# Optimization experiments

Hardware: AMD Instinct MI355X
Metric: run time of the kernel (lower is better)

The kernel has to match this reference:

```python
import jax, jax.numpy as jnp
import numpy as np
import math

B, D_MODEL, SEQ_LEN, EMB_DIM, ORDER = 4, 1024, 4096, 5, 64


def setup_inputs() -> dict:
    key = jax.random.key(0)
    ks = jax.random.split(key, 12)
    L = SEQ_LEN
    # PositionalEmbedding: z = [t, Re(e^{-i f w}), Im(e^{-i f w})]
    t = jnp.linspace(0.0, 1.0, L)[None, :, None]                      # [1,L,1]
    bands = (EMB_DIM - 1) // 2
    t_rescaled = jnp.linspace(0.0, L - 1, L)[None, :, None]           # [1,L,1]
    w = 2 * math.pi * t_rescaled / L
    f = jnp.linspace(1e-4, bands - 1, bands)[None, None]              # [1,1,bands]
    zc = jnp.exp(-1j * f * w.astype(jnp.complex64))                   # [1,L,bands]
    z = jnp.concatenate([t, zc.real, zc.imag], axis=-1)               # [1,L,EMB_DIM]
    # ExponentialModulation deltas (fast_decay_pct=0.3, slow_decay_pct=1.5, target=0.01)
    max_decay = math.log(0.01) / 0.3
    min_decay = math.log(0.01) / 1.5
    deltas = jnp.linspace(min_decay, max_decay, D_MODEL)[None, None]  # [1,1,D]
    s = 0.1  # small init scale for MLP weights
    return {
        "x": jax.random.normal(ks[0], (B, D_MODEL, SEQ_LEN), jnp.float32),
        "L": SEQ_LEN,
        "z": z.astype(jnp.float32),
        "t": t.astype(jnp.float32),
        "deltas": deltas.astype(jnp.float32),
        "W1": jax.random.normal(ks[1], (ORDER, EMB_DIM), jnp.float32) * s,
        "b1": jax.random.normal(ks[2], (ORDER,), jnp.float32) * s,
        "freq": jnp.ones((1, ORDER), jnp.float32),  # Sin freq, w=1
        "W2": jax.random.normal(ks[3], (ORDER, ORDER), jnp.float32) * s,
        "b2": jax.random.normal(ks[4], (ORDER,), jnp.float32) * s,
        "W3": jax.random.normal(ks[5], (ORDER, ORDER), jnp.float32) * s,
        "b3": jax.random.normal(ks[6], (ORDER,), jnp.float32) * s,
        "W4": jax.random.normal(ks[7], (D_MODEL, ORDER), jnp.float32) * s,
        "bias": jax.random.normal(ks[8], (D_MODEL,), jnp.float32),
    }


def reference(x, L, z, t, deltas, W1, b1, freq, W2, b2, W3, b3, W4, bias):
    # --- implicit filter MLP: z [1,L,E] -> k [1,L,D] ---
    zL, tL = z[:, :L], t[:, :L]
    h = jnp.sin(freq * (jnp.einsum('ble,oe->blo', zL, W1) + b1))
    h = jnp.sin(freq * (jnp.einsum('blo,po->blp', h, W2) + b2))
    h = jnp.sin(freq * (jnp.einsum('blo,po->blp', h, W3) + b3))
    h = jnp.einsum('blo,do->bld', h, W4)                # [1,L,D], no bias
    # --- exponential modulation ---
    decay = jnp.exp(-tL * jnp.abs(deltas))              # [1,L,D]
    h = h * decay
    k = h[0].T                                          # [D, L] per-channel filters
    # --- FFT causal conv: irfft(rfft(u)*rfft(k)/n, norm='forward') == plain circular conv on 2L ---
    n = 2 * L
    u_f = jnp.fft.rfft(x, n=n)                          # [B,D,L+1] complex
    k_f = jnp.fft.rfft(k, n=n)                          # [D,L+1]
    y = jnp.fft.irfft(u_f * k_f, n=n)[..., :L]          # [B,D,L]
    out = y + x * bias[:, None]                         # D.unsqueeze(-1) bias term, gelu=False
    return out.astype(x.dtype)
```

## Files before the change

kernel.cpp:

```cpp
#include <hip/hip_runtime.h>
#include <math.h>


#define PAD(i) ((i) + ((i) >> 4))
#define TWO_PI 6.2831853071795864769f

typedef float2 cplx;

__device__ __forceinline__ cplx cmul(cplx a, cplx b) {
    return make_float2(a.x * b.x - a.y * b.y, a.x * b.y + a.y * b.x);
}

__device__ __forceinline__ void dft8(cplx v[8], float sgn) {
    cplx t;
    t = v[1]; v[1] = v[4]; v[4] = t;
    t = v[3]; v[3] = v[6]; v[6] = t;
#pragma unroll
    for (int i = 0; i < 8; i += 2) {
        cplx a = v[i], b = v[i + 1];
        v[i]     = make_float2(a.x + b.x, a.y + b.y);
        v[i + 1] = make_float2(a.x - b.x, a.y - b.y);
    }
#pragma unroll
    for (int i = 0; i < 8; i += 4) {
        cplx a = v[i], b = v[i + 2];
        v[i]     = make_float2(a.x + b.x, a.y + b.y);
        v[i + 2] = make_float2(a.x - b.x, a.y - b.y);
        cplx c1 = v[i + 1], d = v[i + 3];
        cplx dt = make_float2(-sgn * d.y, sgn * d.x);
        v[i + 1] = make_float2(c1.x + dt.x, c1.y + dt.y);
        v[i + 3] = make_float2(c1.x - dt.x, c1.y - dt.y);
    }
    const float C = 0.70710678118654752440f;
    cplx a, b, bt;
    a = v[0]; b = v[4];
    v[0] = make_float2(a.x + b.x, a.y + b.y);
    v[4] = make_float2(a.x - b.x, a.y - b.y);
    a = v[1]; b = v[5]; bt = cmul(b, make_float2(C, sgn * C));
    v[1] = make_float2(a.x + bt.x, a.y + bt.y);
    v[5] = make_float2(a.x - bt.x, a.y - bt.y);
    a = v[2]; b = v[6]; bt = make_float2(-sgn * b.y, sgn * b.x);
    v[2] = make_float2(a.x + bt.x, a.y + bt.y);
    v[6] = make_float2(a.x - bt.x, a.y - bt.y);
    a = v[3]; b = v[7]; bt = cmul(b, make_float2(-C, sgn * C));
    v[3] = make_float2(a.x + bt.x, a.y + bt.y);
    v[7] = make_float2(a.x - bt.x, a.y - bt.y);
}

__device__ __forceinline__ void twiddle_powers(float ang, cplx w[8]) {
    float s, c;
    __sincosf(ang, &s, &c);
    w[1] = make_float2(c, s);
    w[2] = cmul(w[1], w[1]);
    w[3] = cmul(w[2], w[1]);
    w[4] = cmul(w[2], w[2]);
    w[5] = cmul(w[4], w[1]);
    w[6] = cmul(w[3], w[3]);
    w[7] = cmul(w[4], w[3]);
}

template <int NS>
__device__ __forceinline__ void fft_pass_ip(cplx* buf, int j, float sgn) {
    cplx v[8];
#pragma unroll
    for (int r = 0; r < 8; r++) v[r] = buf[PAD(j + (r << 9))];
    if (NS > 1) {
        int jm = j & (NS - 1);
        float ang = sgn * (TWO_PI / (float)(NS * 8)) * (float)jm;
        cplx w[8];
        twiddle_powers(ang, w);
#pragma unroll
        for (int r = 1; r < 8; r++) v[r] = cmul(v[r], w[r]);
    }
    dft8(v, sgn);
    __syncthreads();
    int jm2 = j & (NS - 1);
    int base = ((j & ~(NS - 1)) << 3) + jm2;
#pragma unroll
    for (int r = 0; r < 8; r++) buf[PAD(base + r * NS)] = v[r];
    __syncthreads();
}

__device__ __forceinline__ void fft_pass1_fwd_regs(cplx* buf, int j, const cplx xv[4]) {
    cplx v[8];
#pragma unroll
    for (int r = 0; r < 4; r++) v[r] = xv[r];
#pragma unroll
    for (int r = 4; r < 8; r++) v[r] = make_float2(0.f, 0.f);
    dft8(v, -1.0f);
#pragma unroll
    for (int r = 0; r < 8; r++) buf[PAD(8 * j + r)] = v[r];
    __syncthreads();
}

__global__ __launch_bounds__(256) void mlp_kernel(
    const float* __restrict__ zin, const float* __restrict__ W1,
    const float* __restrict__ b1, const float* __restrict__ freq,
    const float* __restrict__ W2, const float* __restrict__ b2,
    const float* __restrict__ W3, const float* __restrict__ b3,
    float* __restrict__ h3T) {
    __shared__ float hs1[64][64];
    __shared__ float hs2[64][64];
    int tid = threadIdx.x;
    int l = tid & 63, w = tid >> 6;
    int lg = blockIdx.x * 64 + l;

    float zf[5];
#pragma unroll
    for (int e = 0; e < 5; e++) zf[e] = zin[lg * 5 + e];

#pragma unroll
    for (int i = 0; i < 16; i++) {
        int o = w * 16 + i;
        float a = b1[o];
#pragma unroll
        for (int e = 0; e < 5; e++) a += W1[o * 5 + e] * zf[e];
        hs1[o][l] = __sinf(freq[o] * a);
    }
    __syncthreads();

    float acc[16];
#pragma unroll
    for (int i = 0; i < 16; i++) acc[i] = b2[w * 16 + i];
#pragma unroll 8
    for (int o = 0; o < 64; o++) {
        float hv = hs1[o][l];
#pragma unroll
        for (int i = 0; i < 16; i++) acc[i] += W2[(w * 16 + i) * 64 + o] * hv;
    }
#pragma unroll
    for (int i = 0; i < 16; i++)
        hs2[w * 16 + i][l] = __sinf(freq[w * 16 + i] * acc[i]);
    __syncthreads();

#pragma unroll
    for (int i = 0; i < 16; i++) acc[i] = b3[w * 16 + i];
#pragma unroll 8
    for (int o = 0; o < 64; o++) {
        float hv = hs2[o][l];
#pragma unroll
        for (int i = 0; i < 16; i++) acc[i] += W3[(w * 16 + i) * 64 + o] * hv;
    }
#pragma unroll
    for (int i = 0; i < 16; i++)
        h3T[(size_t)(w * 16 + i) * 4096 + lg] = __sinf(freq[w * 16 + i] * acc[i]);
}

__global__ __launch_bounds__(256) void kgemm_kernel(
    const float* __restrict__ h3T, const float* __restrict__ W4,
    const float* __restrict__ tvec, const float* __restrict__ deltas,
    float* __restrict__ kout) {
    int lt = blockIdx.x & 3;
    int dt = blockIdx.x >> 2;
    int l0 = lt * 1024 + threadIdx.x * 4;
    float4 acc[16];
#pragma unroll
    for (int i = 0; i < 16; i++) acc[i] = make_float4(0.f, 0.f, 0.f, 0.f);
#pragma unroll 8
    for (int o = 0; o < 64; o++) {
        float4 h = *(const float4*)(h3T + (size_t)o * 4096 + l0);
#pragma unroll
        for (int i = 0; i < 16; i++) {
            float wv = W4[(size_t)(dt * 16 + i) * 64 + o];
            acc[i].x += wv * h.x; acc[i].y += wv * h.y;
            acc[i].z += wv * h.z; acc[i].w += wv * h.w;
        }
    }
    float4 tl = *(const float4*)(tvec + l0);
#pragma unroll
    for (int i = 0; i < 16; i++) {
        int d = dt * 16 + i;
        float da = fabsf(deltas[d]);
        float4 o;
        o.x = acc[i].x * __expf(-tl.x * da);
        o.y = acc[i].y * __expf(-tl.y * da);
        o.z = acc[i].z * __expf(-tl.z * da);
        o.w = acc[i].w * __expf(-tl.w * da);
        *(float4*)(kout + (size_t)d * 4096 + l0) = o;
    }
}

__global__ __launch_bounds__(512) void filter_fft_kernel(
    const float* __restrict__ kin, float2* __restrict__ Kf) {
    __shared__ cplx buf[4352];
    int d = blockIdx.x, t = threadIdx.x;

    const cplx* k2 = (const cplx*)(kin + (size_t)d * 4096);
    cplx xv[4];
#pragma unroll
    for (int r = 0; r < 4; r++) xv[r] = k2[t + (r << 9)];
    fft_pass1_fwd_regs(buf, t, xv);
    fft_pass_ip<8>(buf, t, -1.0f);
    fft_pass_ip<64>(buf, t, -1.0f);
    fft_pass_ip<512>(buf, t, -1.0f);

    const float scale = 1.0f / 4096.0f;
    float sb, cb;
    __sincosf(-TWO_PI * (float)t * (1.0f / 8192.0f), &sb, &cb);
    cplx wt = make_float2(cb, sb);
    const cplx WC0 = make_float2(1.0f, 0.0f);
    const cplx WC1 = make_float2(0.92387953251128675613f, -0.38268343236508977173f);
    const cplx WC2 = make_float2(0.70710678118654752440f, -0.70710678118654752440f);
    const cplx WC3 = make_float2(0.38268343236508977173f, -0.92387953251128675613f);
    float2* KfRow = Kf + (size_t)d * 4104;
#pragma unroll
    for (int i = 0; i < 4; i++) {
        int k = t + (i << 9);
        cplx wk = (i == 0) ? cmul(wt, WC0) : (i == 1) ? cmul(wt, WC1)
                 : (i == 2) ? cmul(wt, WC2) : cmul(wt, WC3);
        if (k == 0) {
            cplx z0 = buf[PAD(0)];
            KfRow[0]    = make_float2((z0.x + z0.y) * scale, 0.f);
            KfRow[4096] = make_float2((z0.x - z0.y) * scale, 0.f);
            cplx zm = buf[PAD(2048)];
            KfRow[2048] = make_float2(zm.x * scale, -zm.y * scale);
        } else {
            int k2i = 4096 - k;
            cplx Zk = buf[PAD(k)], Zq = buf[PAD(k2i)];
            cplx Fe = make_float2(0.5f * (Zk.x + Zq.x), 0.5f * (Zk.y - Zq.y));
            cplx Fo = make_float2(0.5f * (Zk.y + Zq.y), -0.5f * (Zk.x - Zq.x));
            cplx WFo = cmul(wk, Fo);
            KfRow[k]   = make_float2((Fe.x + WFo.x) * scale, (Fe.y + WFo.y) * scale);
            KfRow[k2i] = make_float2((Fe.x - WFo.x) * scale, -(Fe.y - WFo.y) * scale);
        }
    }
}

__global__ __launch_bounds__(512) void conv_kernel(
    const float* __restrict__ x, const float2* __restrict__ Kf,
    const float* __restrict__ bias, float* __restrict__ out) {
    __shared__ cplx buf[4352];
    int rid = blockIdx.x;
    int d = rid & 1023;
    int t = threadIdx.x;

    const cplx* x2 = (const cplx*)(x + (size_t)rid * 4096);
    cplx xv[4];
#pragma unroll
    for (int r = 0; r < 4; r++) xv[r] = x2[t + (r << 9)];
    fft_pass1_fwd_regs(buf, t, xv);
    fft_pass_ip<8>(buf, t, -1.0f);
    fft_pass_ip<64>(buf, t, -1.0f);
    fft_pass_ip<512>(buf, t, -1.0f);

    const float2* KfRow = Kf + (size_t)d * 4104;
    float sb, cb;
    __sincosf(-TWO_PI * (float)t * (1.0f / 8192.0f), &sb, &cb);
    cplx wt = make_float2(cb, sb);
    const cplx WC0 = make_float2(1.0f, 0.0f);
    const cplx WC1 = make_float2(0.92387953251128675613f, -0.38268343236508977173f);
    const cplx WC2 = make_float2(0.70710678118654752440f, -0.70710678118654752440f);
    const cplx WC3 = make_float2(0.38268343236508977173f, -0.92387953251128675613f);
#pragma unroll
    for (int i = 0; i < 4; i++) {
        int k = t + (i << 9);
        cplx wk = (i == 0) ? cmul(wt, WC0) : (i == 1) ? cmul(wt, WC1)
                 : (i == 2) ? cmul(wt, WC2) : cmul(wt, WC3);
        if (k == 0) {
            cplx z0 = buf[PAD(0)];
            float U0 = z0.x + z0.y;
            float UN = z0.x - z0.y;
            float Y0 = U0 * KfRow[0].x;
            float YN = UN * KfRow[4096].x;
            buf[PAD(0)] = make_float2(0.5f * (Y0 + YN), 0.5f * (Y0 - YN));
            cplx zm = buf[PAD(2048)];
            cplx Um = make_float2(zm.x, -zm.y);
            cplx Ym = cmul(Um, KfRow[2048]);
            buf[PAD(2048)] = make_float2(Ym.x, -Ym.y);
        } else {
            int k2i = 4096 - k;
            cplx Zk = buf[PAD(k)], Zq = buf[PAD(k2i)];
            cplx K1 = KfRow[k], K2 = KfRow[k2i];
            cplx Fe = make_float2(0.5f * (Zk.x + Zq.x), 0.5f * (Zk.y - Zq.y));
            cplx Fo = make_float2(0.5f * (Zk.y + Zq.y), -0.5f * (Zk.x - Zq.x));
            cplx WFo = cmul(wk, Fo);
            cplx U1 = make_float2(Fe.x + WFo.x, Fe.y + WFo.y);
            cplx U2 = make_float2(Fe.x - WFo.x, -(Fe.y - WFo.y));
            cplx Y1 = cmul(U1, K1);
            cplx Y2 = cmul(U2, K2);
            cplx FeY = make_float2(0.5f * (Y1.x + Y2.x), 0.5f * (Y1.y - Y2.y));
            cplx T   = make_float2(0.5f * (Y1.x - Y2.x), 0.5f * (Y1.y + Y2.y));
            cplx FoY = cmul(make_float2(wk.x, -wk.y), T);
            buf[PAD(k)]   = make_float2(FeY.x - FoY.y, FeY.y + FoY.x);
            buf[PAD(k2i)] = make_float2(FeY.x + FoY.y, FoY.x - FeY.y);
        }
    }
    __syncthreads();

    fft_pass_ip<1>(buf, t, 1.0f);
    fft_pass_ip<8>(buf, t, 1.0f);
    fft_pass_ip<64>(buf, t, 1.0f);
    {
        cplx v[8];
#pragma unroll
        for (int r = 0; r < 8; r++) v[r] = buf[PAD(t + (r << 9))];
        float ang = (TWO_PI / 4096.0f) * (float)t;
        cplx w[8];
        twiddle_powers(ang, w);
#pragma unroll
        for (int r = 1; r < 8; r++) v[r] = cmul(v[r], w[r]);
        dft8(v, 1.0f);
        float bd = bias[d];
        cplx* o2 = (cplx*)(out + (size_t)rid * 4096);
#pragma unroll
        for (int r = 0; r < 4; r++) {
            int m = t + (r << 9);
            cplx o;
            o.x = v[r].x + xv[r].x * bd;
            o.y = v[r].y + xv[r].y * bd;
            o2[m] = o;
        }
    }
}

extern "C" void kernel_launch(void* const* d_in, const int* in_sizes, int n_in,
                              void* d_out, int out_size, void* d_ws, size_t ws_size,
                              hipStream_t stream) {
    const float* x      = (const float*)d_in[0];
    const float* zin    = (const float*)d_in[2];
    const float* tvec   = (const float*)d_in[3];
    const float* deltas = (const float*)d_in[4];
    const float* W1     = (const float*)d_in[5];
    const float* b1     = (const float*)d_in[6];
    const float* freq   = (const float*)d_in[7];
    const float* W2     = (const float*)d_in[8];
    const float* b2     = (const float*)d_in[9];
    const float* W3     = (const float*)d_in[10];
    const float* b3     = (const float*)d_in[11];
    const float* W4     = (const float*)d_in[12];
    const float* bias   = (const float*)d_in[13];
    float* out = (float*)d_out;

    float*  h3T = (float*)d_ws;
    float2* Kf  = (float2*)((char*)d_ws + (size_t)64 * 4096 * sizeof(float));
    float* kbuf = out + (size_t)3072 * 4096;

    mlp_kernel<<<64, 256, 0, stream>>>(zin, W1, b1, freq, W2, b2, W3, b3, h3T);
    kgemm_kernel<<<256, 256, 0, stream>>>(h3T, W4, tvec, deltas, kbuf);
    filter_fft_kernel<<<1024, 512, 0, stream>>>(kbuf, Kf);
    conv_kernel<<<4096, 512, 0, stream>>>(x, Kf, bias, out);
}
```

Before: 244.1 us.

## Fuse filter FFT into conv kernel, one block per channel looping over batch

Merges the filter FFT and convolution kernels into one. Each block handles one channel: it computes the filter spectrum once, keeps it in registers, then loops over the four batch rows, prefetching the next row's input while the current row's FFTs run. This removes the Kf round trip through global memory and one kernel launch. The shared-memory FFT addressing is also rewritten to use precomputed padded pointers with constant offsets. In exchange the grid shrinks from 4096 blocks to 1024 and each block runs serially over the batch, which lowers parallelism, and register pressure rises.

```diff
diff --git a/kernel.cpp b/kernel.cpp
--- a/kernel.cpp
+++ b/kernel.cpp
@@ -60,10 +60,11 @@
 }
 
 template <int NS>
-__device__ __forceinline__ void fft_pass_ip(cplx* buf, int j, float sgn) {
+__device__ __forceinline__ void fft_pass_ip(cplx* __restrict__ buf, int j, float sgn) {
+    cplx* rp = buf + (j + (j >> 4));
     cplx v[8];
 #pragma unroll
-    for (int r = 0; r < 8; r++) v[r] = buf[PAD(j + (r << 9))];
+    for (int r = 0; r < 8; r++) v[r] = rp[544 * r];
     if (NS > 1) {
         int jm = j & (NS - 1);
         float ang = sgn * (TWO_PI / (float)(NS * 8)) * (float)jm;
@@ -74,22 +75,31 @@
     }
     dft8(v, sgn);
     __syncthreads();
-    int jm2 = j & (NS - 1);
-    int base = ((j & ~(NS - 1)) << 3) + jm2;
-#pragma unroll
-    for (int r = 0; r < 8; r++) buf[PAD(base + r * NS)] = v[r];
-    __syncthreads();
-}
-
-__device__ __forceinline__ void fft_pass1_fwd_regs(cplx* buf, int j, const cplx xv[4]) {
+    int base = ((j & ~(NS - 1)) << 3) + (j & (NS - 1));
+    cplx* wp = buf + (base + (base >> 4));
+#pragma unroll
+    for (int r = 0; r < 8; r++) {
+        const int off = (NS == 1) ? r
+                      : (NS == 8) ? (8 * r + (r >> 1))
+                      : (NS == 64) ? (68 * r)
+                      : (544 * r);
+        wp[off] = v[r];
+    }
+    __syncthreads();
+}
+
+__device__ __forceinline__ void fft_pass1_fwd_regs(cplx* __restrict__ buf, int j,
+                                                   const cplx xv[4]) {
     cplx v[8];
 #pragma unroll
     for (int r = 0; r < 4; r++) v[r] = xv[r];
 #pragma unroll
     for (int r = 4; r < 8; r++) v[r] = make_float2(0.f, 0.f);
     dft8(v, -1.0f);
-#pragma unroll
-    for (int r = 0; r < 8; r++) buf[PAD(8 * j + r)] = v[r];
+    int b8 = 8 * j;
+    cplx* wp = buf + (b8 + (b8 >> 4));
+#pragma unroll
+    for (int r = 0; r < 8; r++) wp[r] = v[r];
     __syncthreads();
 }
 
@@ -180,136 +190,132 @@
     }
 }
 
-__global__ __launch_bounds__(512) void filter_fft_kernel(
-    const float* __restrict__ kin, float2* __restrict__ Kf) {
+__global__ __launch_bounds__(512) void convf_kernel(
+    const float* __restrict__ x, const float* __restrict__ kin,
+    const float* __restrict__ bias, float* __restrict__ out) {
     __shared__ cplx buf[4352];
-    int d = blockIdx.x, t = threadIdx.x;
-
-    const cplx* k2 = (const cplx*)(kin + (size_t)d * 4096);
-    cplx xv[4];
-#pragma unroll
-    for (int r = 0; r < 4; r++) xv[r] = k2[t + (r << 9)];
-    fft_pass1_fwd_regs(buf, t, xv);
-    fft_pass_ip<8>(buf, t, -1.0f);
-    fft_pass_ip<64>(buf, t, -1.0f);
-    fft_pass_ip<512>(buf, t, -1.0f);
-
-    const float scale = 1.0f / 4096.0f;
+    int d = blockIdx.x;
+    int t = threadIdx.x;
+
     float sb, cb;
     __sincosf(-TWO_PI * (float)t * (1.0f / 8192.0f), &sb, &cb);
-    cplx wt = make_float2(cb, sb);
-    const cplx WC0 = make_float2(1.0f, 0.0f);
-    const cplx WC1 = make_float2(0.92387953251128675613f, -0.38268343236508977173f);
-    const cplx WC2 = make_float2(0.70710678118654752440f, -0.70710678118654752440f);
-    const cplx WC3 = make_float2(0.38268343236508977173f, -0.92387953251128675613f);
-    float2* KfRow = Kf + (size_t)d * 4104;
+    cplx wk[4];
+    wk[0] = make_float2(cb, sb);
+    wk[1] = cmul(wk[0], make_float2(0.92387953251128675613f, -0.38268343236508977173f));
+    wk[2] = cmul(wk[0], make_float2(0.70710678118654752440f, -0.70710678118654752440f));
+    wk[3] = cmul(wk[0], make_float2(0.38268343236508977173f, -0.92387953251128675613f));
+
+    cplx* rb  = buf + (t + (t >> 4));
+    cplx* qb2 = buf + (((4096 - t) + ((4096 - t) >> 4)) - 1632);
+
+    {
+        const cplx* k2 = (const cplx*)(kin + (size_t)d * 4096);
+        cplx kv[4];
+#pragma unroll
+        for (int r = 0; r < 4; r++) kv[r] = k2[t + (r << 9)];
+        fft_pass1_fwd_regs(buf, t, kv);
+        fft_pass_ip<8>(buf, t, -1.0f);
+        fft_pass_ip<64>(buf, t, -1.0f);
+        fft_pass_ip<512>(buf, t, -1.0f);
+    }
+    const float scale = 1.0f / 4096.0f;
+    cplx Kk[4], Kq[4], Km = make_float2(0.f, 0.f);
 #pragma unroll
     for (int i = 0; i < 4; i++) {
-        int k = t + (i << 9);
-        cplx wk = (i == 0) ? cmul(wt, WC0) : (i == 1) ? cmul(wt, WC1)
-                 : (i == 2) ? cmul(wt, WC2) : cmul(wt, WC3);
-        if (k == 0) {
-            cplx z0 = buf[PAD(0)];
-            KfRow[0]    = make_float2((z0.x + z0.y) * scale, 0.f);
-            KfRow[4096] = make_float2((z0.x - z0.y) * scale, 0.f);
+        if (t == 0 && i == 0) {
+            cplx z0 = buf[0];
+            Kk[0] = make_float2((z0.x + z0.y) * scale, (z0.x - z0.y) * scale);
             cplx zm = buf[PAD(2048)];
-            KfRow[2048] = make_float2(zm.x * scale, -zm.y * scale);
+            Km = make_float2(zm.x * scale, -zm.y * scale);
+            Kq[0] = make_float2(0.f, 0.f);
         } else {
-            int k2i = 4096 - k;
-            cplx Zk = buf[PAD(k)], Zq = buf[PAD(k2i)];
+            cplx Zk = rb[544 * i];
+            cplx Zq = qb2[544 * (3 - i)];
             cplx Fe = make_float2(0.5f * (Zk.x + Zq.x), 0.5f * (Zk.y - Zq.y));
             cplx Fo = make_float2(0.5f * (Zk.y + Zq.y), -0.5f * (Zk.x - Zq.x));
-            cplx WFo = cmul(wk, Fo);
-            KfRow[k]   = make_float2((Fe.x + WFo.x) * scale, (Fe.y + WFo.y) * scale);
-            KfRow[k2i] = make_float2((Fe.x - WFo.x) * scale, -(Fe.y - WFo.y) * scale);
-        }
-    }
-}
-
-__global__ __launch_bounds__(512) void conv_kernel(
-    const float* __restrict__ x, const float2* __restrict__ Kf,
-    const float* __restrict__ bias, float* __restrict__ out) {
-    __shared__ cplx buf[4352];
-    int rid = blockIdx.x;
-    int d = rid & 1023;
-    int t = threadIdx.x;
-
-    const cplx* x2 = (const cplx*)(x + (size_t)rid * 4096);
-    cplx xv[4];
-#pragma unroll
-    for (int r = 0; r < 4; r++) xv[r] = x2[t + (r << 9)];
-    fft_pass1_fwd_regs(buf, t, xv);
-    fft_pass_ip<8>(buf, t, -1.0f);
-    fft_pass_ip<64>(buf, t, -1.0f);
-    fft_pass_ip<512>(buf, t, -1.0f);
-
-    const float2* KfRow = Kf + (size_t)d * 4104;
-    float sb, cb;
-    __sincosf(-TWO_PI * (float)t * (1.0f / 8192.0f), &sb, &cb);
-    cplx wt = make_float2(cb, sb);
-    const cplx WC0 = make_float2(1.0f, 0.0f);
-    const cplx WC1 = make_float2(0.92387953251128675613f, -0.38268343236508977173f);
-    const cplx WC2 = make_float2(0.70710678118654752440f, -0.70710678118654752440f);
-    const cplx WC3 = make_float2(0.38268343236508977173f, -0.92387953251128675613f);
-#pragma unroll
-    for (int i = 0; i < 4; i++) {
-        int k = t + (i << 9);
-        cplx wk = (i == 0) ? cmul(wt, WC0) : (i == 1) ? cmul(wt, WC1)
-                 : (i == 2) ? cmul(wt, WC2) : cmul(wt, WC3);
-        if (k == 0) {
-            cplx z0 = buf[PAD(0)];
-            float U0 = z0.x + z0.y;
-            float UN = z0.x - z0.y;
-            float Y0 = U0 * KfRow[0].x;
-            float YN = UN * KfRow[4096].x;
-            buf[PAD(0)] = make_float2(0.5f * (Y0 + YN), 0.5f * (Y0 - YN));
-            cplx zm = buf[PAD(2048)];
-            cplx Um = make_float2(zm.x, -zm.y);
-            cplx Ym = cmul(Um, KfRow[2048]);
-            buf[PAD(2048)] = make_float2(Ym.x, -Ym.y);
-        } else {
-            int k2i = 4096 - k;
-            cplx Zk = buf[PAD(k)], Zq = buf[PAD(k2i)];
-            cplx K1 = KfRow[k], K2 = KfRow[k2i];
-            cplx Fe = make_float2(0.5f * (Zk.x + Zq.x), 0.5f * (Zk.y - Zq.y));
-            cplx Fo = make_float2(0.5f * (Zk.y + Zq.y), -0.5f * (Zk.x - Zq.x));
-            cplx WFo = cmul(wk, Fo);
-            cplx U1 = make_float2(Fe.x + WFo.x, Fe.y + WFo.y);
-            cplx U2 = make_float2(Fe.x - WFo.x, -(Fe.y - WFo.y));
-            cplx Y1 = cmul(U1, K1);
-            cplx Y2 = cmul(U2, K2);
-            cplx FeY = make_float2(0.5f * (Y1.x + Y2.x), 0.5f * (Y1.y - Y2.y));
-            cplx T   = make_float2(0.5f * (Y1.x - Y2.x), 0.5f * (Y1.y + Y2.y));
-            cplx FoY = cmul(make_float2(wk.x, -wk.y), T);
-            buf[PAD(k)]   = make_float2(FeY.x - FoY.y, FeY.y + FoY.x);
-            buf[PAD(k2i)] = make_float2(FeY.x + FoY.y, FoY.x - FeY.y);
-        }
-    }
-    __syncthreads();
-
-    fft_pass_ip<1>(buf, t, 1.0f);
-    fft_pass_ip<8>(buf, t, 1.0f);
-    fft_pass_ip<64>(buf, t, 1.0f);
+            cplx WFo = cmul(wk[i], Fo);
+            Kk[i] = make_float2((Fe.x + WFo.x) * scale, (Fe.y + WFo.y) * scale);
+            Kq[i] = make_float2((Fe.x - WFo.x) * scale, -(Fe.y - WFo.y) * scale);
+        }
+    }
+
+    float bd = bias[d];
+    cplx xv[4], xn[4];
     {
-        cplx v[8];
-#pragma unroll
-        for (int r = 0; r < 8; r++) v[r] = buf[PAD(t + (r << 9))];
-        float ang = (TWO_PI / 4096.0f) * (float)t;
-        cplx w[8];
-        twiddle_powers(ang, w);
-#pragma unroll
-        for (int r = 1; r < 8; r++) v[r] = cmul(v[r], w[r]);
-        dft8(v, 1.0f);
-        float bd = bias[d];
-        cplx* o2 = (cplx*)(out + (size_t)rid * 4096);
-#pragma unroll
-        for (int r = 0; r < 4; r++) {
-            int m = t + (r << 9);
-            cplx o;
-            o.x = v[r].x + xv[r].x * bd;
-            o.y = v[r].y + xv[r].y * bd;
-            o2[m] = o;
-        }
+        const cplx* xr = (const cplx*)(x + (size_t)d * 4096);
+#pragma unroll
+        for (int r = 0; r < 4; r++) xv[r] = xr[t + (r << 9)];
+    }
+
+#pragma unroll 1
+    for (int b = 0; b < 4; b++) {
+        __syncthreads();
+        fft_pass1_fwd_regs(buf, t, xv);
+        if (b < 3) {
+            const cplx* xr = (const cplx*)(x + ((size_t)(b + 1) * 1024 + d) * 4096);
+#pragma unroll
+            for (int r = 0; r < 4; r++) xn[r] = xr[t + (r << 9)];
+        }
+        fft_pass_ip<8>(buf, t, -1.0f);
+        fft_pass_ip<64>(buf, t, -1.0f);
+        fft_pass_ip<512>(buf, t, -1.0f);
+
+#pragma unroll
+        for (int i = 0; i < 4; i++) {
+            if (t == 0 && i == 0) {
+                cplx z0 = buf[0];
+                float U0 = z0.x + z0.y;
+                float UN = z0.x - z0.y;
+                float Y0 = U0 * Kk[0].x;
+                float YN = UN * Kk[0].y;
+                buf[0] = make_float2(0.5f * (Y0 + YN), 0.5f * (Y0 - YN));
+                cplx zm = buf[PAD(2048)];
+                cplx Um = make_float2(zm.x, -zm.y);
+                cplx Ym = cmul(Um, Km);
+                buf[PAD(2048)] = make_float2(Ym.x, -Ym.y);
+            } else {
+                cplx Zk = rb[544 * i];
+                cplx Zq = qb2[544 * (3 - i)];
+                cplx Fe = make_float2(0.5f * (Zk.x + Zq.x), 0.5f * (Zk.y - Zq.y));
+                cplx Fo = make_float2(0.5f * (Zk.y + Zq.y), -0.5f * (Zk.x - Zq.x));
+                cplx WFo = cmul(wk[i], Fo);
+                cplx U1 = make_float2(Fe.x + WFo.x, Fe.y + WFo.y);
+                cplx U2 = make_float2(Fe.x - WFo.x, -(Fe.y - WFo.y));
+                cplx Y1 = cmul(U1, Kk[i]);
+                cplx Y2 = cmul(U2, Kq[i]);
+                cplx FeY = make_float2(0.5f * (Y1.x + Y2.x), 0.5f * (Y1.y - Y2.y));
+                cplx T   = make_float2(0.5f * (Y1.x - Y2.x), 0.5f * (Y1.y + Y2.y));
+                cplx FoY = cmul(make_float2(wk[i].x, -wk[i].y), T);
+                rb[544 * i]        = make_float2(FeY.x - FoY.y, FeY.y + FoY.x);
+                qb2[544 * (3 - i)] = make_float2(FeY.x + FoY.y, FoY.x - FeY.y);
+            }
+        }
+        __syncthreads();
+
+        fft_pass_ip<1>(buf, t, 1.0f);
+        fft_pass_ip<8>(buf, t, 1.0f);
+        fft_pass_ip<64>(buf, t, 1.0f);
+        {
+            cplx v[8];
+#pragma unroll
+            for (int r = 0; r < 8; r++) v[r] = rb[544 * r];
+            float ang = (TWO_PI / 4096.0f) * (float)t;
+            cplx w[8];
+            twiddle_powers(ang, w);
+#pragma unroll
+            for (int r = 1; r < 8; r++) v[r] = cmul(v[r], w[r]);
+            dft8(v, 1.0f);
+            cplx* o2 = (cplx*)(out + ((size_t)b * 1024 + d) * 4096);
+#pragma unroll
+            for (int r = 0; r < 4; r++) {
+                cplx o;
+                o.x = v[r].x + xv[r].x * bd;
+                o.y = v[r].y + xv[r].y * bd;
+                o2[t + (r << 9)] = o;
+            }
+        }
+#pragma unroll
+        for (int r = 0; r < 4; r++) xv[r] = xn[r];
     }
 }
 
@@ -331,12 +337,10 @@
     const float* bias   = (const float*)d_in[13];
     float* out = (float*)d_out;
 
-    float*  h3T = (float*)d_ws;
-    float2* Kf  = (float2*)((char*)d_ws + (size_t)64 * 4096 * sizeof(float));
-    float* kbuf = out + (size_t)3072 * 4096;
+    float* h3T  = (float*)d_ws;
+    float* kbuf = (float*)((char*)d_ws + (size_t)64 * 4096 * sizeof(float));
 
     mlp_kernel<<<64, 256, 0, stream>>>(zin, W1, b1, freq, W2, b2, W3, b3, h3T);
     kgemm_kernel<<<256, 256, 0, stream>>>(h3T, W4, tvec, deltas, kbuf);
-    filter_fft_kernel<<<1024, 512, 0, stream>>>(kbuf, Kf);
-    conv_kernel<<<4096, 512, 0, stream>>>(x, Kf, bias, out);
-}
+    convf_kernel<<<1024, 512, 0, stream>>>(x, kbuf, bias, out);
+}
```

New measurement: 271.8 us. 1.11x slower.
